# Performance work log

Measured on AMD Instinct MI355X. Metric: run time of the kernel, lower is better.

The kernel has to match this reference:

```python
import jax, jax.numpy as jnp
import numpy as np

F = 256   # num_features
H = 64    # hidden_dim
DEPTH = 5 # -> 3 hidden-to-hidden layers
B = 16384


def setup_inputs() -> dict:
    key = jax.random.key(0)
    ks = jax.random.split(key, 7)
    x = jax.random.normal(ks[0], (B, F), dtype=jnp.float32)
    # per-feature params, batched over F (torch default init ~ U(-1/sqrt(fan_in), 1/sqrt(fan_in)))
    W1 = jax.random.uniform(ks[1], (F, H), jnp.float32, -1.0, 1.0)          # fan_in = 1
    b1 = jax.random.uniform(ks[2], (F, H), jnp.float32, -1.0, 1.0)
    lim = 1.0 / np.sqrt(H)
    Wh = jax.random.uniform(ks[3], (DEPTH - 2, F, H, H), jnp.float32, -lim, lim)
    bh = jax.random.uniform(ks[4], (DEPTH - 2, F, H), jnp.float32, -lim, lim)
    Wo = jax.random.uniform(ks[5], (F, H), jnp.float32, -lim, lim)
    bo = jax.random.uniform(ks[6], (F,), jnp.float32, -lim, lim)
    return {"x": x, "W1": W1, "b1": b1, "Wh": Wh, "bh": bh, "Wo": Wo, "bo": bo}


def reference(x, W1, b1, Wh, bh, Wo, bo):
    # first layer: scalar input per feature -> hidden. h: [B, F, H]
    h = x[:, :, None] * W1[None, :, :] + b1[None, :, :]
    # (depth-2) hidden layers: ReLU then per-feature GEMM (dropout p=0 -> no-op)
    for l in range(Wh.shape[0]):
        h = jnp.einsum('bfh,fhk->bfk', jax.nn.relu(h), Wh[l]) + bh[l][None]
    # output layer: hidden -> scalar per feature, then sum over features
    feats = jnp.einsum('bfh,fh->bf', jax.nn.relu(h), Wo) + bo[None, :]
    return feats.sum(axis=1)  # [B]
```

## Files before the change

### kernel.cpp

```cpp
#include <hip/hip_runtime.h>

typedef _Float16 f16;
typedef f16    f16x2 __attribute__((ext_vector_type(2)));
typedef f16    f16x8 __attribute__((ext_vector_type(8)));
typedef __fp16 fp16x2 __attribute__((ext_vector_type(2)));
typedef float  f32x4 __attribute__((ext_vector_type(4)));

#define NF 256
#define NH 64
#define NL 3
#define NB 4
#define NWAVE 4
#define MT (NB * 16 * NWAVE)
#define NTHR (NWAVE * 64)
#define WFRAG (NH * NH)

union U2 { f16x8 v8; f16x2 h[4]; };


__device__ __forceinline__ f16x2 pkmax(float a, float b) {
    fp16x2 p = __builtin_amdgcn_cvt_pkrtz(a, b);
    fp16x2 z = {(__fp16)0.f, (__fp16)0.f};
    p = __builtin_elementwise_max(p, z);
    return __builtin_bit_cast(f16x2, p);
}

__global__ __launch_bounds__(256) void presplit_w(
    const float* __restrict__ Wh, f16* __restrict__ wsHi)
{
    __shared__ float wld[NH * NH];
    const int lf = blockIdx.x;
    const int t  = threadIdx.x;
    const float* __restrict__ src = Wh + (size_t)lf * WFRAG;
#pragma unroll
    for (int i = 0; i < 4; ++i)
        *(f32x4*)&wld[(i * 256 + t) * 4] = *(const f32x4*)&src[(i * 256 + t) * 4];
    __syncthreads();
#pragma unroll
    for (int g2 = 0; g2 < 2; ++g2) {
        const int g  = g2 * 256 + t;
        const int ln = g & 63, ks = (g >> 6) & 1, mt = g >> 7;
        const int cl = ln & 15, gr = ln >> 4;
        const int m  = mt * 16 + cl;
        f16x8 hi;
#pragma unroll
        for (int jj = 0; jj < 8; ++jj) {
            const int u = 32 * ks + 16 * (jj >> 2) + 4 * gr + (jj & 3);
            hi[jj] = (f16)wld[u * NH + m];
        }
        *(f16x8*)&wsHi[((size_t)lf * 512 + g) * 8] = hi;
    }
}

template <bool PRE>
__global__ __launch_bounds__(NTHR, 4) void permlp_v13(
    const float* __restrict__ x,
    const float* __restrict__ W1,
    const float* __restrict__ b1,
    const float* __restrict__ Wh,
    const float* __restrict__ bh,
    const float* __restrict__ Wo,
    const float* __restrict__ bo,
    const f16* __restrict__ wsHi,
    float* __restrict__ out,
    int nby)
{
    const int nwg  = NF * nby;
    const int q    = nwg >> 3;
    const int bid  = blockIdx.x;
    const int wgid = (bid & 7) * q + (bid >> 3);
    const int f    = wgid / nby;
    const int by   = wgid - f * nby;

    const int tid = threadIdx.x;
    const int wv  = tid >> 6;
    const int ln  = tid & 63;
    const int cl  = ln & 15;
    const int gr  = ln >> 4;
    const int gb0 = by * MT + wv * (NB * 16);

    auto loadW = [&](const f16* __restrict__ baseH, const float* __restrict__ Wl,
                     int mt, f16x8 (&A)[2]) {
#pragma unroll
        for (int ks = 0; ks < 2; ++ks) {
            if constexpr (PRE) {
                A[ks] = *(const f16x8*)&baseH[(size_t)((mt * 2 + ks) * 64 + ln) * 8];
            } else {
                const int m = mt * 16 + cl;
                f16x8 hi8;
#pragma unroll
                for (int j = 0; j < 8; ++j) {
                    const int u = 32 * ks + 16 * (j >> 2) + 4 * gr + (j & 3);
                    hi8[j] = (f16)Wl[(size_t)u * NH + m];
                }
                A[ks] = hi8;
            }
        }
    };

    U2 HA[NB][2], HB[NB][2];
    {
        float xv[NB];
#pragma unroll
        for (int bt = 0; bt < NB; ++bt)
            xv[bt] = x[(size_t)(gb0 + bt * 16 + cl) * NF + f];
        const float* __restrict__ w1 = W1 + f * NH;
        const float* __restrict__ bb = b1 + f * NH;
#pragma unroll
        for (int ks = 0; ks < 2; ++ks)
#pragma unroll
            for (int jq = 0; jq < 2; ++jq) {
                const int ub = 32 * ks + 16 * jq + 4 * gr;
                const f32x4 w4 = *(const f32x4*)&w1[ub];
                const f32x4 b4 = *(const f32x4*)&bb[ub];
#pragma unroll
                for (int bt = 0; bt < NB; ++bt) {
                    float v0 = fmaf(xv[bt], w4[0], b4[0]);
                    float v1 = fmaf(xv[bt], w4[1], b4[1]);
                    float v2 = fmaf(xv[bt], w4[2], b4[2]);
                    float v3 = fmaf(xv[bt], w4[3], b4[3]);
                    HA[bt][ks].h[jq * 2]     = pkmax(v0, v1);
                    HA[bt][ks].h[jq * 2 + 1] = pkmax(v2, v3);
                }
            }
    }

    auto hidden = [&](U2 (&I)[NB][2], U2 (&O)[NB][2], const int l) {
        const f16* __restrict__ baseH = PRE ? wsHi + (size_t)(l * NF + f) * 4096 : nullptr;
        const float* __restrict__ Wl  = Wh + (size_t)(l * NF + f) * WFRAG;
        const float* __restrict__ bl  = bh + (size_t)(l * NF + f) * NH;
        f16x8 WA[2][2];
        loadW(baseH, Wl, 0, WA[0]);
#pragma unroll
        for (int mt = 0; mt < 4; ++mt) {
            if (mt < 3)
                loadW(baseH, Wl, mt + 1, WA[(mt + 1) & 1]);
            const f32x4 bias4 = *(const f32x4*)&bl[mt * 16 + gr * 4];
            f32x4 acc[NB];
#pragma unroll
            for (int bt = 0; bt < NB; ++bt) acc[bt] = bias4;
#pragma unroll
            for (int ks = 0; ks < 2; ++ks)
#pragma unroll
                for (int bt = 0; bt < NB; ++bt)
                    acc[bt] = __builtin_amdgcn_mfma_f32_16x16x32_f16(WA[mt & 1][ks], I[bt][ks].v8, acc[bt], 0, 0, 0);
#pragma unroll
            for (int bt = 0; bt < NB; ++bt) {
                O[bt][mt >> 1].h[(mt & 1) * 2]     = pkmax(acc[bt][0], acc[bt][1]);
                O[bt][mt >> 1].h[(mt & 1) * 2 + 1] = pkmax(acc[bt][2], acc[bt][3]);
            }
        }
    };

    hidden(HA, HB, 0);
    hidden(HB, HA, 1);

    float souts[NB] = {0.f, 0.f, 0.f, 0.f};
    {
        const int l = NL - 1;
        const f16* __restrict__ baseH = PRE ? wsHi + (size_t)(l * NF + f) * 4096 : nullptr;
        const float* __restrict__ Wl  = Wh + (size_t)(l * NF + f) * WFRAG;
        const float* __restrict__ bl  = bh + (size_t)(l * NF + f) * NH;
        f16x8 WA[2][2];
        loadW(baseH, Wl, 0, WA[0]);
#pragma unroll
        for (int mt = 0; mt < 4; ++mt) {
            if (mt < 3)
                loadW(baseH, Wl, mt + 1, WA[(mt + 1) & 1]);
            const f32x4 bias4 = *(const f32x4*)&bl[mt * 16 + gr * 4];
            f32x4 acc[NB];
#pragma unroll
            for (int bt = 0; bt < NB; ++bt) acc[bt] = bias4;
#pragma unroll
            for (int ks = 0; ks < 2; ++ks)
#pragma unroll
                for (int bt = 0; bt < NB; ++bt)
                    acc[bt] = __builtin_amdgcn_mfma_f32_16x16x32_f16(WA[mt & 1][ks], HA[bt][ks].v8, acc[bt], 0, 0, 0);
            const f32x4 wov4 = *(const f32x4*)&Wo[f * NH + mt * 16 + gr * 4];
#pragma unroll
            for (int bt = 0; bt < NB; ++bt)
#pragma unroll
                for (int i = 0; i < 4; ++i)
                    souts[bt] = fmaf(fmaxf(acc[bt][i], 0.f), wov4[i], souts[bt]);
        }
    }

    const float bof = bo[f];
#pragma unroll
    for (int bt = 0; bt < NB; ++bt) {
        float s = souts[bt];
        s += __shfl_xor(s, 16, 64);
        s += __shfl_xor(s, 32, 64);
        if (ln < 16)
            atomicAdd(&out[gb0 + bt * 16 + ln], s + bof);
    }
}

extern "C" void kernel_launch(void* const* d_in, const int* in_sizes, int n_in,
                              void* d_out, int out_size, void* d_ws, size_t ws_size,
                              hipStream_t stream)
{
    const float* x  = (const float*)d_in[0];
    const float* W1 = (const float*)d_in[1];
    const float* b1 = (const float*)d_in[2];
    const float* Wh = (const float*)d_in[3];
    const float* bh = (const float*)d_in[4];
    const float* Wo = (const float*)d_in[5];
    const float* bo = (const float*)d_in[6];
    float* out = (float*)d_out;

    const int B   = in_sizes[0] / NF;
    const int nby = B / MT;

    hipMemsetAsync(out, 0, (size_t)out_size * sizeof(float), stream);

    const size_t planeElems = (size_t)NL * NF * WFRAG;
    const size_t needW      = planeElems * sizeof(f16);
    dim3 grid(NF * nby);

    if (ws_size >= needW) {
        f16* wsHi = (f16*)d_ws;
        presplit_w<<<NL * NF, 256, 0, stream>>>(Wh, wsHi);
        permlp_v13<true><<<grid, dim3(NTHR), 0, stream>>>(
            x, W1, b1, Wh, bh, Wo, bo, wsHi, out, nby);
    } else {
        permlp_v13<false><<<grid, dim3(NTHR), 0, stream>>>(
            x, W1, b1, Wh, bh, Wo, bo, nullptr, out, nby);
    }
}
```

Before: 139.3 us.

## Shrink batch tile, raise occupancy, pack first/output layers to fp16 packed math

```diff
diff --git a/kernel.cpp b/kernel.cpp
--- a/kernel.cpp
+++ b/kernel.cpp
@@ -2,6 +2,7 @@
 
 typedef _Float16 f16;
 typedef f16    f16x2 __attribute__((ext_vector_type(2)));
+typedef f16    f16x4 __attribute__((ext_vector_type(4)));
 typedef f16    f16x8 __attribute__((ext_vector_type(8)));
 typedef __fp16 fp16x2 __attribute__((ext_vector_type(2)));
 typedef float  f32x4 __attribute__((ext_vector_type(4)));
@@ -9,13 +10,15 @@
 #define NF 256
 #define NH 64
 #define NL 3
-#define NB 4
+#define NB 3
 #define NWAVE 4
 #define MT (NB * 16 * NWAVE)
 #define NTHR (NWAVE * 64)
 #define WFRAG (NH * NH)
 
-union U2 { f16x8 v8; f16x2 h[4]; };
+union U2  { f16x8 v8; f16x2 h[4]; };
+union WB1 { f16x8 v8; fp16x2 p[4]; };
+union WO4 { f16x4 v4; fp16x2 p[2]; };
 
 
 __device__ __forceinline__ f16x2 pkmax(float a, float b) {
@@ -24,9 +27,22 @@
     p = __builtin_elementwise_max(p, z);
     return __builtin_bit_cast(f16x2, p);
 }
+__device__ __forceinline__ f16x2 pkfmarelu(fp16x2 x, fp16x2 w, fp16x2 b) {
+    fp16x2 p = __builtin_elementwise_fma(x, w, b);
+    fp16x2 z = {(__fp16)0.f, (__fp16)0.f};
+    p = __builtin_elementwise_max(p, z);
+    return __builtin_bit_cast(f16x2, p);
+}
+__device__ __forceinline__ float dot2(f16x2 a, fp16x2 b, float c) {
+#if __has_builtin(__builtin_amdgcn_fdot2)
+    return __builtin_amdgcn_fdot2(__builtin_bit_cast(fp16x2, a), b, c, false);
+#else
+    return fmaf((float)a[0], (float)b[0], fmaf((float)a[1], (float)b[1], c));
+#endif
+}
 
 __global__ __launch_bounds__(256) void presplit_w(
-    const float* __restrict__ Wh, f16* __restrict__ wsHi)
+    const float* __restrict__ Wh, f16* __restrict__ wsWh)
 {
     __shared__ float wld[NH * NH];
     const int lf = blockIdx.x;
@@ -48,12 +64,39 @@
             const int u = 32 * ks + 16 * (jj >> 2) + 4 * gr + (jj & 3);
             hi[jj] = (f16)wld[u * NH + m];
         }
-        *(f16x8*)&wsHi[((size_t)lf * 512 + g) * 8] = hi;
+        *(f16x8*)&wsWh[((size_t)lf * 512 + g) * 8] = hi;
+    }
+}
+
+__global__ __launch_bounds__(64) void prepack_small(
+    const float* __restrict__ W1, const float* __restrict__ b1,
+    const float* __restrict__ Wo,
+    f16* __restrict__ wsW1B, f16* __restrict__ wsWo)
+{
+    const int f = blockIdx.x;
+    const int t = threadIdx.x;
+    if (t < 16) {
+        const int gr = t & 3, jq = (t >> 2) & 1, ks = t >> 3;
+        const int ub = 32 * ks + 16 * jq + 4 * gr;
+        f16x8 o;
+#pragma unroll
+        for (int i = 0; i < 4; ++i) o[i]     = (f16)W1[f * NH + ub + i];
+#pragma unroll
+        for (int i = 0; i < 4; ++i) o[4 + i] = (f16)b1[f * NH + ub + i];
+        *(f16x8*)&wsW1B[((size_t)f * 16 + t) * 8] = o;
+    } else if (t < 32) {
+        const int s = t - 16;
+        const int mt = s >> 2, gr = s & 3;
+        f16x4 o;
+#pragma unroll
+        for (int i = 0; i < 4; ++i)
+            o[i] = (f16)Wo[f * NH + mt * 16 + gr * 4 + i];
+        *(f16x4*)&wsWo[((size_t)f * 16 + s) * 4] = o;
     }
 }
 
 template <bool PRE>
-__global__ __launch_bounds__(NTHR, 4) void permlp_v13(
+__global__ __launch_bounds__(NTHR, 5) void permlp_v14(
     const float* __restrict__ x,
     const float* __restrict__ W1,
     const float* __restrict__ b1,
@@ -61,9 +104,11 @@
     const float* __restrict__ bh,
     const float* __restrict__ Wo,
     const float* __restrict__ bo,
-    const f16* __restrict__ wsHi,
+    const f16* __restrict__ wsWh,
+    const f16* __restrict__ wsW1B,
+    const f16* __restrict__ wsWo,
     float* __restrict__ out,
-    int nby)
+    int nby, int Btot)
 {
     const int nwg  = NF * nby;
     const int q    = nwg >> 3;
@@ -100,41 +145,55 @@
 
     U2 HA[NB][2], HB[NB][2];
     {
-        float xv[NB];
-#pragma unroll
-        for (int bt = 0; bt < NB; ++bt)
-            xv[bt] = x[(size_t)(gb0 + bt * 16 + cl) * NF + f];
-        const float* __restrict__ w1 = W1 + f * NH;
-        const float* __restrict__ bb = b1 + f * NH;
-#pragma unroll
-        for (int ks = 0; ks < 2; ++ks)
-#pragma unroll
-            for (int jq = 0; jq < 2; ++jq) {
-                const int ub = 32 * ks + 16 * jq + 4 * gr;
-                const f32x4 w4 = *(const f32x4*)&w1[ub];
-                const f32x4 b4 = *(const f32x4*)&bb[ub];
-#pragma unroll
-                for (int bt = 0; bt < NB; ++bt) {
-                    float v0 = fmaf(xv[bt], w4[0], b4[0]);
-                    float v1 = fmaf(xv[bt], w4[1], b4[1]);
-                    float v2 = fmaf(xv[bt], w4[2], b4[2]);
-                    float v3 = fmaf(xv[bt], w4[3], b4[3]);
-                    HA[bt][ks].h[jq * 2]     = pkmax(v0, v1);
-                    HA[bt][ks].h[jq * 2 + 1] = pkmax(v2, v3);
+        fp16x2 xx[NB];
+#pragma unroll
+        for (int bt = 0; bt < NB; ++bt) {
+            const int row = gb0 + bt * 16 + cl;
+            const float xv = (row < Btot) ? x[(size_t)row * NF + f] : 0.f;
+            xx[bt] = __builtin_amdgcn_cvt_pkrtz(xv, xv);
+        }
+        if constexpr (PRE) {
+            const f16* __restrict__ wb1 = wsW1B + (size_t)f * 128;
+#pragma unroll
+            for (int ks = 0; ks < 2; ++ks)
+#pragma unroll
+                for (int jq = 0; jq < 2; ++jq) {
+                    WB1 wb;
+                    wb.v8 = *(const f16x8*)&wb1[(size_t)((ks * 2 + jq) * 4 + gr) * 8];
+#pragma unroll
+                    for (int bt = 0; bt < NB; ++bt) {
+                        HA[bt][ks].h[jq * 2]     = pkfmarelu(xx[bt], wb.p[0], wb.p[2]);
+                        HA[bt][ks].h[jq * 2 + 1] = pkfmarelu(xx[bt], wb.p[1], wb.p[3]);
+                    }
                 }
-            }
+        } else {
+            const float* __restrict__ w1 = W1 + f * NH;
+            const float* __restrict__ bb = b1 + f * NH;
+#pragma unroll
+            for (int ks = 0; ks < 2; ++ks)
+#pragma unroll
+                for (int jq = 0; jq < 2; ++jq) {
+                    const int ub = 32 * ks + 16 * jq + 4 * gr;
+                    const f32x4 w4 = *(const f32x4*)&w1[ub];
+                    const f32x4 b4 = *(const f32x4*)&bb[ub];
+#pragma unroll
+                    for (int bt = 0; bt < NB; ++bt) {
+                        float xv = (float)xx[bt][0];
+                        HA[bt][ks].h[jq * 2]     = pkmax(fmaf(xv, w4[0], b4[0]), fmaf(xv, w4[1], b4[1]));
+                        HA[bt][ks].h[jq * 2 + 1] = pkmax(fmaf(xv, w4[2], b4[2]), fmaf(xv, w4[3], b4[3]));
+                    }
+                }
+        }
     }
 
     auto hidden = [&](U2 (&I)[NB][2], U2 (&O)[NB][2], const int l) {
-        const f16* __restrict__ baseH = PRE ? wsHi + (size_t)(l * NF + f) * 4096 : nullptr;
+        const f16* __restrict__ baseH = PRE ? wsWh + (size_t)(l * NF + f) * 4096 : nullptr;
         const float* __restrict__ Wl  = Wh + (size_t)(l * NF + f) * WFRAG;
         const float* __restrict__ bl  = bh + (size_t)(l * NF + f) * NH;
-        f16x8 WA[2][2];
-        loadW(baseH, Wl, 0, WA[0]);
 #pragma unroll
         for (int mt = 0; mt < 4; ++mt) {
-            if (mt < 3)
-                loadW(baseH, Wl, mt + 1, WA[(mt + 1) & 1]);
+            f16x8 WA[2];
+            loadW(baseH, Wl, mt, WA);
             const f32x4 bias4 = *(const f32x4*)&bl[mt * 16 + gr * 4];
             f32x4 acc[NB];
 #pragma unroll
@@ -143,7 +202,7 @@
             for (int ks = 0; ks < 2; ++ks)
 #pragma unroll
                 for (int bt = 0; bt < NB; ++bt)
-                    acc[bt] = __builtin_amdgcn_mfma_f32_16x16x32_f16(WA[mt & 1][ks], I[bt][ks].v8, acc[bt], 0, 0, 0);
+                    acc[bt] = __builtin_amdgcn_mfma_f32_16x16x32_f16(WA[ks], I[bt][ks].v8, acc[bt], 0, 0, 0);
 #pragma unroll
             for (int bt = 0; bt < NB; ++bt) {
                 O[bt][mt >> 1].h[(mt & 1) * 2]     = pkmax(acc[bt][0], acc[bt][1]);
@@ -155,18 +214,18 @@
     hidden(HA, HB, 0);
     hidden(HB, HA, 1);
 
-    float souts[NB] = {0.f, 0.f, 0.f, 0.f};
+    float souts[NB];
+#pragma unroll
+    for (int bt = 0; bt < NB; ++bt) souts[bt] = 0.f;
     {
         const int l = NL - 1;
-        const f16* __restrict__ baseH = PRE ? wsHi + (size_t)(l * NF + f) * 4096 : nullptr;
+        const f16* __restrict__ baseH = PRE ? wsWh + (size_t)(l * NF + f) * 4096 : nullptr;
         const float* __restrict__ Wl  = Wh + (size_t)(l * NF + f) * WFRAG;
         const float* __restrict__ bl  = bh + (size_t)(l * NF + f) * NH;
-        f16x8 WA[2][2];
-        loadW(baseH, Wl, 0, WA[0]);
 #pragma unroll
         for (int mt = 0; mt < 4; ++mt) {
-            if (mt < 3)
-                loadW(baseH, Wl, mt + 1, WA[(mt + 1) & 1]);
+            f16x8 WA[2];
+            loadW(baseH, Wl, mt, WA);
             const f32x4 bias4 = *(const f32x4*)&bl[mt * 16 + gr * 4];
             f32x4 acc[NB];
 #pragma unroll
@@ -175,13 +234,25 @@
             for (int ks = 0; ks < 2; ++ks)
 #pragma unroll
                 for (int bt = 0; bt < NB; ++bt)
-                    acc[bt] = __builtin_amdgcn_mfma_f32_16x16x32_f16(WA[mt & 1][ks], HA[bt][ks].v8, acc[bt], 0, 0, 0);
-            const f32x4 wov4 = *(const f32x4*)&Wo[f * NH + mt * 16 + gr * 4];
-#pragma unroll
-            for (int bt = 0; bt < NB; ++bt)
-#pragma unroll
-                for (int i = 0; i < 4; ++i)
-                    souts[bt] = fmaf(fmaxf(acc[bt][i], 0.f), wov4[i], souts[bt]);
+                    acc[bt] = __builtin_amdgcn_mfma_f32_16x16x32_f16(WA[ks], HA[bt][ks].v8, acc[bt], 0, 0, 0);
+            if constexpr (PRE) {
+                WO4 wo;
+                wo.v4 = *(const f16x4*)&wsWo[((size_t)f * 16 + mt * 4 + gr) * 4];
+#pragma unroll
+                for (int bt = 0; bt < NB; ++bt) {
+                    f16x2 p01 = pkmax(acc[bt][0], acc[bt][1]);
+                    f16x2 p23 = pkmax(acc[bt][2], acc[bt][3]);
+                    souts[bt] = dot2(p01, wo.p[0], souts[bt]);
+                    souts[bt] = dot2(p23, wo.p[1], souts[bt]);
+                }
+            } else {
+                const f32x4 wov4 = *(const f32x4*)&Wo[f * NH + mt * 16 + gr * 4];
+#pragma unroll
+                for (int bt = 0; bt < NB; ++bt)
+#pragma unroll
+                    for (int i = 0; i < 4; ++i)
+                        souts[bt] = fmaf(fmaxf(acc[bt][i], 0.f), wov4[i], souts[bt]);
+            }
         }
     }
 
@@ -191,8 +262,9 @@
         float s = souts[bt];
         s += __shfl_xor(s, 16, 64);
         s += __shfl_xor(s, 32, 64);
-        if (ln < 16)
-            atomicAdd(&out[gb0 + bt * 16 + ln], s + bof);
+        const int row = gb0 + bt * 16 + ln;
+        if (ln < 16 && row < Btot)
+            atomicAdd(&out[row], s + bof);
     }
 }
 
@@ -210,21 +282,26 @@
     float* out = (float*)d_out;
 
     const int B   = in_sizes[0] / NF;
-    const int nby = B / MT;
+    const int nby = (B + MT - 1) / MT;
 
     hipMemsetAsync(out, 0, (size_t)out_size * sizeof(float), stream);
 
-    const size_t planeElems = (size_t)NL * NF * WFRAG;
-    const size_t needW      = planeElems * sizeof(f16);
+    const size_t whElems  = (size_t)NL * NF * WFRAG;
+    const size_t w1bElems = (size_t)NF * 16 * 8;
+    const size_t woElems  = (size_t)NF * 16 * 4;
+    const size_t needW    = (whElems + w1bElems + woElems) * sizeof(f16);
     dim3 grid(NF * nby);
 
     if (ws_size >= needW) {
-        f16* wsHi = (f16*)d_ws;
-        presplit_w<<<NL * NF, 256, 0, stream>>>(Wh, wsHi);
-        permlp_v13<true><<<grid, dim3(NTHR), 0, stream>>>(
-            x, W1, b1, Wh, bh, Wo, bo, wsHi, out, nby);
+        f16* wsWh  = (f16*)d_ws;
+        f16* wsW1B = wsWh + whElems;
+        f16* wsWo  = wsW1B + w1bElems;
+        presplit_w<<<NL * NF, 256, 0, stream>>>(Wh, wsWh);
+        prepack_small<<<NF, 64, 0, stream>>>(W1, b1, Wo, wsW1B, wsWo);
+        permlp_v14<true><<<grid, dim3(NTHR), 0, stream>>>(
+            x, W1, b1, Wh, bh, Wo, bo, wsWh, wsW1B, wsWo, out, nby, B);
     } else {
-        permlp_v13<false><<<grid, dim3(NTHR), 0, stream>>>(
-            x, W1, b1, Wh, bh, Wo, bo, nullptr, out, nby);
-    }
-}
+        permlp_v14<false><<<grid, dim3(NTHR), 0, stream>>>(
+            x, W1, b1, Wh, bh, Wo, bo, nullptr, nullptr, nullptr, out, nby, B);
+    }
+}
```

New measurement: 162.3 us. 16.5% more time.
